# Optimization experiments

Hardware: AMD Instinct MI355X
Metric: run time of the kernel (lower is better)

## Reference

```python
import jax, jax.numpy as jnp
import numpy as np

B, S, D, H = 2, 2048, 1024, 16
DK = D // H


def setup_inputs() -> dict:
    key = jax.random.key(0)
    ks = jax.random.split(key, 12)
    k_init = 1.0 / np.sqrt(D)  # torch Linear-style uniform bound used in the module
    def lin(kw, kb):
        W = jax.random.uniform(kw, (D, D), jnp.float32, -k_init, k_init)
        b = jax.random.uniform(kb, (D,), jnp.float32, -k_init, k_init)
        return W, b
    Wq, bq = lin(ks[0], ks[1])
    Wk, bk = lin(ks[2], ks[3])
    Wv, bv = lin(ks[4], ks[5])
    Wo, bo = lin(ks[6], ks[7])
    query = jax.random.normal(ks[8], (B, S, D), jnp.float32)
    key_t = jax.random.normal(ks[9], (B, S, D), jnp.float32)
    value = jax.random.normal(ks[10], (B, S, D), jnp.float32)
    # causal mask: 1 where attention allowed, 0 where blocked
    mask = jnp.broadcast_to(jnp.tril(jnp.ones((S, S), jnp.int32)), (B, S, S))
    return {"query": query, "key": key_t, "value": value, "mask": mask,
            "Wq": Wq, "bq": bq, "Wk": Wk, "bk": bk, "Wv": Wv, "bv": bv,
            "Wo": Wo, "bo": bo}


def reference(query, key, value, mask, Wq, bq, Wk, bk, Wv, bv, Wo, bo):
    bs = query.shape[0]
    # projections: torch Linear computes x @ W.T + b
    def proj(x, W, b):
        y = x @ W.T + b                      # [B, S, D]
        return y.reshape(bs, -1, H, DK).transpose(0, 2, 1, 3)  # [B, H, S, DK]
    q = proj(query, Wq, bq)
    k = proj(key, Wk, bk)
    v = proj(value, Wv, bv)
    scale = 1.0 / np.sqrt(DK).astype(np.float32)
    scores = jnp.einsum('bhqd,bhkd->bhqk', q, k) * scale  # [B, H, S, S]
    scores = jnp.where(mask[:, None, :, :] == 0, jnp.float32(-1e9), scores)
    p_attn = jax.nn.softmax(scores, axis=-1)
    # dropout omitted (eval mode / deterministic reference)
    x = jnp.einsum('bhqk,bhkd->bhqd', p_attn, v)          # [B, H, S, DK]
    x = x.transpose(0, 2, 1, 3).reshape(bs, -1, D)        # [B, S, D]
    return x @ Wo.T + bo
```

## Files before the change

kernel.cpp:

```cpp
#include <hip/hip_runtime.h>
#include <hip/hip_bf16.h>
#include <math.h>

#define BB 2
#define SS 2048
#define DD 1024
#define HH 16
#define DKK 64
#define NT (BB * SS)

typedef __attribute__((ext_vector_type(8))) short short8;
typedef __attribute__((ext_vector_type(4))) float f32x4;
typedef __attribute__((ext_vector_type(16))) float f32x16;

__device__ __forceinline__ unsigned short f2b(float x) {
    __hip_bfloat16 h = __float2bfloat16(x);
    unsigned short u; __builtin_memcpy(&u, &h, 2); return u;
}
__device__ __forceinline__ unsigned pack2(float a, float b) {
    return (unsigned)f2b(a) | ((unsigned)f2b(b) << 16);
}

struct CastAll {
    const float* src[7];
    unsigned short* dst[7];
};

__global__ __launch_bounds__(256)
void cast_all(CastAll a) {
    const int tid0 = blockIdx.x * 256 + threadIdx.x;
    const int stride = gridDim.x * 256;
    #pragma unroll
    for (int s = 0; s < 7; ++s) {
        const int n4 = (s < 3) ? (NT * DD / 4) : (DD * DD / 4);
        const float* __restrict__ src = a.src[s];
        unsigned short* __restrict__ dst = a.dst[s];
        for (int i = tid0; i < n4; i += stride) {
            const float4 v = reinterpret_cast<const float4*>(src)[i];
            ushort4 o;
            o.x = f2b(v.x); o.y = f2b(v.y); o.z = f2b(v.z); o.w = f2b(v.w);
            reinterpret_cast<ushort4*>(dst)[i] = o;
        }
    }
}

template <int MODE>
__device__ __forceinline__ void gemm_body(const unsigned short* __restrict__ A,
                                          const unsigned short* __restrict__ W,
                                          const float* __restrict__ bias,
                                          void* __restrict__ Cv,
                                          int bm, int bn, int N, int K) {
    __shared__ __align__(16) unsigned char sA[128 * 128];
    __shared__ __align__(16) unsigned char sB[128 * 128];

    const int tid = threadIdx.x;
    const int l = tid & 63;
    const int w = tid >> 6;
    const int wr = w >> 1, wc = w & 1;
    const int g = l >> 4, li = l & 15;
    const int lrow = l >> 3;
    const int lcol = (l & 7) * 8;

    f32x4 acc[4][4];
    #pragma unroll
    for (int i = 0; i < 4; ++i)
        #pragma unroll
        for (int jj = 0; jj < 4; ++jj) {
            acc[i][jj][0] = 0.f; acc[i][jj][1] = 0.f;
            acc[i][jj][2] = 0.f; acc[i][jj][3] = 0.f;
        }

    for (int kt = 0; kt < K; kt += 64) {
        #pragma unroll
        for (int c = 0; c < 4; ++c) {
            const int row0 = w * 32 + c * 8;
            const unsigned short* gA = A + (size_t)(bm + row0 + lrow) * K + kt + lcol;
            __builtin_amdgcn_global_load_lds(
                (const __attribute__((address_space(1))) unsigned int*)gA,
                (__attribute__((address_space(3))) unsigned int*)&sA[row0 * 128],
                16, 0, 0);
            const unsigned short* gB = W + (size_t)(bn + row0 + lrow) * K + kt + lcol;
            __builtin_amdgcn_global_load_lds(
                (const __attribute__((address_space(1))) unsigned int*)gB,
                (__attribute__((address_space(3))) unsigned int*)&sB[row0 * 128],
                16, 0, 0);
        }
        __syncthreads();

        #pragma unroll
        for (int kb = 0; kb < 2; ++kb) {
            const int chb = (g + kb * 4) * 16;
            short8 af[4], bfr[4];
            #pragma unroll
            for (int mi = 0; mi < 4; ++mi)
                af[mi] = *reinterpret_cast<const short8*>(
                    &sA[(wr * 64 + mi * 16 + li) * 128 + chb]);
            #pragma unroll
            for (int ni = 0; ni < 4; ++ni)
                bfr[ni] = *reinterpret_cast<const short8*>(
                    &sB[(wc * 64 + ni * 16 + li) * 128 + chb]);
            #pragma unroll
            for (int mi = 0; mi < 4; ++mi)
                #pragma unroll
                for (int ni = 0; ni < 4; ++ni)
                    acc[mi][ni] = __builtin_amdgcn_mfma_f32_16x16x32_bf16(af[mi], bfr[ni], acc[mi][ni], 0, 0, 0);
        }
        __syncthreads();
    }

    #pragma unroll
    for (int ni = 0; ni < 4; ++ni) {
        const int col = bn + wc * 64 + ni * 16 + li;
        const float bv = bias[col];
        if constexpr (MODE == 2) {
            const int hh = col >> 6, d = col & 63;
            const int bb = bm >> 11;
            unsigned short* vt = (unsigned short*)Cv;
            #pragma unroll
            for (int mi = 0; mi < 4; ++mi) {
                const int srow0 = (bm & (SS - 1)) + wr * 64 + mi * 16 + g * 4;
                ushort4 pk4;
                pk4.x = f2b(acc[mi][ni][0] + bv);
                pk4.y = f2b(acc[mi][ni][1] + bv);
                pk4.z = f2b(acc[mi][ni][2] + bv);
                pk4.w = f2b(acc[mi][ni][3] + bv);
                *reinterpret_cast<ushort4*>(
                    &vt[(size_t)((bb * 16 + hh) * 64 + d) * SS + srow0]) = pk4;
            }
        } else {
            #pragma unroll
            for (int mi = 0; mi < 4; ++mi) {
                const int row0 = bm + wr * 64 + mi * 16 + g * 4;
                #pragma unroll
                for (int r = 0; r < 4; ++r) {
                    const float v = acc[mi][ni][r] + bv;
                    if constexpr (MODE == 0)
                        ((unsigned short*)Cv)[(size_t)(row0 + r) * N + col] = f2b(v);
                    else
                        ((float*)Cv)[(size_t)(row0 + r) * N + col] = v;
                }
            }
        }
    }
}

struct QKVArgs {
    const unsigned short* A[3];
    const unsigned short* W[3];
    const float* bias[3];
    unsigned short* C[2];
    unsigned short* vt;
};

__global__ __launch_bounds__(256)
void gemm_qkv(QKVArgs args) {
    const int bid = blockIdx.x;
    const int i = (bid & 7) * 96 + (bid >> 3);
    const int z = i >> 8;
    const int rem = i & 255;
    const int by = rem >> 3, bx = rem & 7;
    if (z == 2)
        gemm_body<2>(args.A[2], args.W[2], args.bias[2], args.vt, by * 128, bx * 128, DD, DD);
    else
        gemm_body<0>(args.A[z], args.W[z], args.bias[z], args.C[z], by * 128, bx * 128, DD, DD);
}

__global__ __launch_bounds__(256)
void gemm_out(const unsigned short* __restrict__ A, const unsigned short* __restrict__ W,
              const float* __restrict__ bias, float* __restrict__ C) {
    const int bid = blockIdx.x;
    const int i = (bid & 7) * 32 + (bid >> 3);
    const int by = i >> 3, bx = i & 7;
    gemm_body<1>(A, W, bias, C, by * 128, bx * 128, DD, DD);
}

__global__ __launch_bounds__(256)
void attn_mfma(const unsigned short* __restrict__ Q,
               const unsigned short* __restrict__ Kb,
               const unsigned short* __restrict__ Vt,
               unsigned short* __restrict__ X) {
    __shared__ __align__(16) unsigned char sK[128 * 128];
    __shared__ __align__(16) unsigned char sV[64 * 256];

    const int bid = blockIdx.x;
    const int xcd = bid & 7;
    const int idx = bid >> 3;
    const int j   = 15 - (idx >> 2);
    const int bh  = xcd * 4 + (idx & 3);
    const int b = bh >> 4, h = bh & 15;

    const int tid = threadIdx.x, l = tid & 63, w = tid >> 6;
    const int h5 = l >> 5, q5 = l & 31;
    const int col0 = h * DKK;
    const int qbase = j * 128 + w * 32;
    const float scale = 0.125f;

    short8 qf[4];
    {
        const unsigned short* qp = Q + (size_t)(b * SS + qbase + q5) * DD + col0;
        #pragma unroll
        for (int s = 0; s < 4; ++s)
            qf[s] = *reinterpret_cast<const short8*>(&qp[(2 * s + h5) * 8]);
    }

    f32x16 accO[2];
    #pragma unroll
    for (int d0 = 0; d0 < 2; ++d0)
        #pragma unroll
        for (int r = 0; r < 16; ++r) accO[d0][r] = 0.f;
    float m = -INFINITY, lsum = 0.f;

    for (int kt = 0; kt <= j; ++kt) {
        {
            const unsigned short* krow = Kb + (size_t)(b * SS + kt * 128) * DD + col0;
            #pragma unroll
            for (int i = 0; i < 4; ++i) {
                const int row = w * 32 + i * 8 + (l >> 3);
                const int cj = l & 7;
                __builtin_amdgcn_global_load_lds(
                    (const __attribute__((address_space(1))) unsigned int*)
                        (krow + (size_t)row * DD + ((cj ^ (row & 7)) << 3)),
                    (__attribute__((address_space(3))) unsigned int*)&sK[w * 4096 + i * 1024],
                    16, 0, 0);
            }
            const unsigned short* vrow = Vt + (size_t)(bh * 64) * SS + kt * 128;
            #pragma unroll
            for (int i = 0; i < 4; ++i) {
                const int d = w * 16 + i * 4 + (l >> 4);
                const int cj = l & 15;
                __builtin_amdgcn_global_load_lds(
                    (const __attribute__((address_space(1))) unsigned int*)
                        (vrow + (size_t)d * SS + ((cj ^ (d & 15)) << 3)),
                    (__attribute__((address_space(3))) unsigned int*)&sV[w * 4096 + i * 1024],
                    16, 0, 0);
            }
        }
        __syncthreads();

        const bool diag = (kt == j);
        const int fact = diag ? w : 3;

        f32x16 accS[4];
        __builtin_amdgcn_s_setprio(1);
        #pragma unroll
        for (int f = 0; f < 4; ++f) {
            if (f <= fact) {
                #pragma unroll
                for (int r = 0; r < 16; ++r) accS[f][r] = 0.f;
                #pragma unroll
                for (int s = 0; s < 4; ++s) {
                    const short8 kf = *reinterpret_cast<const short8*>(
                        &sK[(f * 32 + q5) * 128 + (((2 * s + h5) ^ (q5 & 7)) << 4)]);
                    accS[f] = __builtin_amdgcn_mfma_f32_32x32x16_bf16(kf, qf[s], accS[f], 0, 0, 0);
                }
            }
        }
        __builtin_amdgcn_s_setprio(0);

        float tmax = -INFINITY;
        #pragma unroll
        for (int f = 0; f < 4; ++f) {
            if (f <= fact) {
                #pragma unroll
                for (int r = 0; r < 16; ++r) {
                    float v = accS[f][r] * scale;
                    if (diag && f == w) {
                        const int off = (r & 3) + 8 * (r >> 2) + 4 * h5;
                        if (off > q5) v = -3e38f;
                    }
                    accS[f][r] = v;
                    tmax = fmaxf(tmax, v);
                }
            }
        }
        tmax = fmaxf(tmax, __shfl_xor(tmax, 32));

        if (!__all(tmax <= m)) {
            const float mn = fmaxf(m, tmax);
            const float corr = __expf(m - mn);
            lsum *= corr;
            #pragma unroll
            for (int r = 0; r < 16; ++r) {
                const int rowloc = (r & 3) + 8 * (r >> 2) + 4 * h5;
                const float cr = __shfl(corr, rowloc | (l & 32));
                accO[0][r] *= cr;
                accO[1][r] *= cr;
            }
            m = mn;
        }

        float psum = 0.f;
        unsigned pk[32];
        #pragma unroll
        for (int f = 0; f < 4; ++f) {
            if (f <= fact) {
                #pragma unroll
                for (int i2 = 0; i2 < 8; ++i2) {
                    const float pa = __expf(accS[f][2 * i2] - m);
                    const float pb = __expf(accS[f][2 * i2 + 1] - m);
                    psum += pa + pb;
                    pk[f * 8 + i2] = pack2(pa, pb);
                }
            }
        }
        psum += __shfl_xor(psum, 32);
        lsum += psum;

        const int smax = diag ? (2 * w + 1) : 7;
        __builtin_amdgcn_s_setprio(1);
        #pragma unroll
        for (int s = 0; s < 8; ++s) {
            if (s <= smax) {
                const int fb = (s >> 1) * 8 + (s & 1) * 4;
                const unsigned sendA = h5 ? pk[fb + 0] : pk[fb + 2];
                const unsigned sendB = h5 ? pk[fb + 1] : pk[fb + 3];
                const unsigned rA = __shfl_xor(sendA, 32);
                const unsigned rB = __shfl_xor(sendB, 32);
                union { unsigned u[4]; short8 s8; } pf;
                pf.u[0] = h5 ? rA : pk[fb + 0];
                pf.u[1] = h5 ? rB : pk[fb + 1];
                pf.u[2] = h5 ? pk[fb + 2] : rA;
                pf.u[3] = h5 ? pk[fb + 3] : rB;
                #pragma unroll
                for (int d0 = 0; d0 < 2; ++d0) {
                    const short8 vf = *reinterpret_cast<const short8*>(
                        &sV[(d0 * 32 + q5) * 256 + (((2 * s + h5) ^ (q5 & 15)) << 4)]);
                    accO[d0] = __builtin_amdgcn_mfma_f32_32x32x16_bf16(pf.s8, vf, accO[d0], 0, 0, 0);
                }
            }
        }
        __builtin_amdgcn_s_setprio(0);
        __syncthreads();
    }

    const float invl = 1.f / lsum;
    #pragma unroll
    for (int r = 0; r < 16; ++r) {
        const int rowloc = (r & 3) + 8 * (r >> 2) + 4 * h5;
        const float iv = __shfl(invl, rowloc | (l & 32));
        const size_t qrow = (size_t)(b * SS + qbase + rowloc) * DD + col0;
        #pragma unroll
        for (int d0 = 0; d0 < 2; ++d0)
            X[qrow + d0 * 32 + q5] = f2b(accO[d0][r] * iv);
    }
}

extern "C" void kernel_launch(void* const* d_in, const int* in_sizes, int n_in,
                              void* d_out, int out_size, void* d_ws, size_t ws_size,
                              hipStream_t stream) {
    const float* query = (const float*)d_in[0];
    const float* key   = (const float*)d_in[1];
    const float* value = (const float*)d_in[2];
    const float* Wq = (const float*)d_in[4];
    const float* bq = (const float*)d_in[5];
    const float* Wk = (const float*)d_in[6];
    const float* bk = (const float*)d_in[7];
    const float* Wv = (const float*)d_in[8];
    const float* bv = (const float*)d_in[9];
    const float* Wo = (const float*)d_in[10];
    const float* bo = (const float*)d_in[11];
    float* out = (float*)d_out;

    unsigned short* ws16 = (unsigned short*)d_ws;
    const size_t TOK = (size_t)NT * DD;
    const size_t WSZ = (size_t)DD * DD;
    unsigned short* qb  = ws16;
    unsigned short* kb  = ws16 + TOK;
    unsigned short* vt  = ws16 + 2 * TOK;
    unsigned short* xb  = ws16 + 3 * TOK;
    unsigned short* xqb = ws16 + 4 * TOK;
    unsigned short* xkb = ws16 + 5 * TOK;
    unsigned short* xvb = ws16 + 6 * TOK;
    unsigned short* wqb = ws16 + 7 * TOK;
    unsigned short* wkb = wqb + WSZ;
    unsigned short* wvb = wkb + WSZ;
    unsigned short* wob = wvb + WSZ;

    CastAll ca;
    ca.src[0] = query; ca.dst[0] = xqb;
    ca.src[1] = key;   ca.dst[1] = xkb;
    ca.src[2] = value; ca.dst[2] = xvb;
    ca.src[3] = Wq;    ca.dst[3] = wqb;
    ca.src[4] = Wk;    ca.dst[4] = wkb;
    ca.src[5] = Wv;    ca.dst[5] = wvb;
    ca.src[6] = Wo;    ca.dst[6] = wob;
    cast_all<<<2048, 256, 0, stream>>>(ca);

    QKVArgs args;
    args.A[0] = xqb; args.A[1] = xkb; args.A[2] = xvb;
    args.W[0] = wqb; args.W[1] = wkb; args.W[2] = wvb;
    args.bias[0] = bq; args.bias[1] = bk; args.bias[2] = bv;
    args.C[0] = qb;  args.C[1] = kb;  args.vt = vt;
    gemm_qkv<<<768, 256, 0, stream>>>(args);

    attn_mfma<<<512, 256, 0, stream>>>(qb, kb, vt, xb);

    gemm_out<<<256, 256, 0, stream>>>(xb, wob, bo, out);
}
```

Before: 273.8 us.

## Split causal attention into KV chunks with a separate merge kernel

The single causal attention kernel is replaced by a split-KV scheme. Each query tile's KV range is cut into chunks of up to four tiles, giving 1280 work items of roughly equal size instead of 512 blocks whose work grows with query position. Each chunk writes an unnormalized bf16 partial output plus its row max and sum to workspace that is reused from the cast buffers. A new merge kernel then rescales and combines the partials into X. This aims to fix load imbalance and tail effects across CUs, at the cost of an extra launch, extra global traffic for partials, and bf16 rounding of the unnormalized partials. It also adds a minimum-occupancy hint to the launch bounds.

```diff
diff --git a/kernel.cpp b/kernel.cpp
--- a/kernel.cpp
+++ b/kernel.cpp
@@ -8,6 +8,8 @@
 #define HH 16
 #define DKK 64
 #define NT (BB * SS)
+#define NCHUNK 1280
+#define CPB 40
 
 typedef __attribute__((ext_vector_type(8))) short short8;
 typedef __attribute__((ext_vector_type(4))) float f32x4;
@@ -16,6 +18,9 @@
 __device__ __forceinline__ unsigned short f2b(float x) {
     __hip_bfloat16 h = __float2bfloat16(x);
     unsigned short u; __builtin_memcpy(&u, &h, 2); return u;
+}
+__device__ __forceinline__ float b2f(unsigned short u) {
+    union { unsigned u; float f; } c; c.u = ((unsigned)u) << 16; return c.f;
 }
 __device__ __forceinline__ unsigned pack2(float a, float b) {
     return (unsigned)f2b(a) | ((unsigned)f2b(b) << 16);
@@ -174,19 +179,25 @@
     gemm_body<1>(A, W, bias, C, by * 128, bx * 128, DD, DD);
 }
 
-__global__ __launch_bounds__(256)
-void attn_mfma(const unsigned short* __restrict__ Q,
+__global__ __launch_bounds__(256, 3)
+void attn_part(const unsigned short* __restrict__ Q,
                const unsigned short* __restrict__ Kb,
                const unsigned short* __restrict__ Vt,
-               unsigned short* __restrict__ X) {
+               unsigned short* __restrict__ Opart,
+               float* __restrict__ ML) {
     __shared__ __align__(16) unsigned char sK[128 * 128];
     __shared__ __align__(16) unsigned char sV[64 * 256];
 
     const int bid = blockIdx.x;
     const int xcd = bid & 7;
-    const int idx = bid >> 3;
-    const int j   = 15 - (idx >> 2);
-    const int bh  = xcd * 4 + (idx & 3);
+    const int slot = bid >> 3;
+    const int bh = xcd * 4 + slot / CPB;
+    const int cidx = (CPB - 1) - (slot % CPB);
+    int j = 0, rem = cidx;
+    while (rem >= ((j >> 2) + 1)) { rem -= (j >> 2) + 1; ++j; }
+    const int c = rem;
+    const int kt0 = 4 * c;
+    const int kt1 = (4 * c + 3 < j) ? (4 * c + 3) : j;
     const int b = bh >> 4, h = bh & 15;
 
     const int tid = threadIdx.x, l = tid & 63, w = tid >> 6;
@@ -210,7 +221,7 @@
         for (int r = 0; r < 16; ++r) accO[d0][r] = 0.f;
     float m = -INFINITY, lsum = 0.f;
 
-    for (int kt = 0; kt <= j; ++kt) {
+    for (int kt = kt0; kt <= kt1; ++kt) {
         {
             const unsigned short* krow = Kb + (size_t)(b * SS + kt * 128) * DD + col0;
             #pragma unroll
@@ -333,15 +344,78 @@
         __syncthreads();
     }
 
-    const float invl = 1.f / lsum;
     #pragma unroll
     for (int r = 0; r < 16; ++r) {
         const int rowloc = (r & 3) + 8 * (r >> 2) + 4 * h5;
-        const float iv = __shfl(invl, rowloc | (l & 32));
-        const size_t qrow = (size_t)(b * SS + qbase + rowloc) * DD + col0;
+        const int qrow = w * 32 + rowloc;
         #pragma unroll
         for (int d0 = 0; d0 < 2; ++d0)
-            X[qrow + d0 * 32 + q5] = f2b(accO[d0][r] * iv);
+            Opart[(size_t)bid * 8192 + qrow * 64 + d0 * 32 + q5] = f2b(accO[d0][r]);
+    }
+    if (h5 == 0) {
+        ML[bid * 256 + w * 32 + q5] = m;
+        ML[bid * 256 + 128 + w * 32 + q5] = lsum;
+    }
+}
+
+__global__ __launch_bounds__(256)
+void attn_merge(const unsigned short* __restrict__ Opart,
+                const float* __restrict__ ML,
+                unsigned short* __restrict__ X) {
+    const int bid = blockIdx.x;
+    const int xcd = bid & 7, s = bid >> 3;
+    const int bh = xcd * 4 + (s >> 4);
+    const int j = s & 15;
+    const int b = bh >> 4, h = bh & 15;
+    const int a = j >> 2, bb = j & 3;
+    const int offj = (a + 1) * (2 * a + bb);
+    const int nc = a + 1;
+    const int tid = threadIdx.x;
+    const int q = tid >> 1, dh = (tid & 1) * 32;
+
+    float mc[4], lc[4];
+    float M = -INFINITY;
+    #pragma unroll
+    for (int cc = 0; cc < 4; ++cc) {
+        if (cc < nc) {
+            const int slot = (bh & 3) * CPB + (CPB - 1) - (offj + cc);
+            const int gb = slot * 8 + xcd;
+            mc[cc] = ML[gb * 256 + q];
+            lc[cc] = ML[gb * 256 + 128 + q];
+            M = fmaxf(M, mc[cc]);
+        } else { mc[cc] = -INFINITY; lc[cc] = 0.f; }
+    }
+
+    float L = 0.f;
+    float o[32];
+    #pragma unroll
+    for (int e = 0; e < 32; ++e) o[e] = 0.f;
+    #pragma unroll
+    for (int cc = 0; cc < 4; ++cc) {
+        if (cc < nc) {
+            const int slot = (bh & 3) * CPB + (CPB - 1) - (offj + cc);
+            const int gb = slot * 8 + xcd;
+            const float wgt = __expf(mc[cc] - M);
+            L += lc[cc] * wgt;
+            const unsigned short* op = Opart + (size_t)gb * 8192 + q * 64 + dh;
+            #pragma unroll
+            for (int v = 0; v < 4; ++v) {
+                const short8 pv = *reinterpret_cast<const short8*>(&op[v * 8]);
+                #pragma unroll
+                for (int e = 0; e < 8; ++e)
+                    o[v * 8 + e] += wgt * b2f((unsigned short)pv[e]);
+            }
+        }
+    }
+
+    const float inv = 1.f / L;
+    unsigned short* xp = X + (size_t)(b * SS + j * 128 + q) * DD + h * DKK + dh;
+    #pragma unroll
+    for (int v = 0; v < 4; ++v) {
+        short8 o8;
+        #pragma unroll
+        for (int e = 0; e < 8; ++e) o8[e] = (short)f2b(o[v * 8 + e] * inv);
+        *reinterpret_cast<short8*>(&xp[v * 8]) = o8;
     }
 }
 
@@ -376,6 +450,9 @@
     unsigned short* wvb = wkb + WSZ;
     unsigned short* wob = wvb + WSZ;
 
+    unsigned short* opart = xqb;
+    float* ml = (float*)wqb;
+
     CastAll ca;
     ca.src[0] = query; ca.dst[0] = xqb;
     ca.src[1] = key;   ca.dst[1] = xkb;
@@ -393,7 +470,8 @@
     args.C[0] = qb;  args.C[1] = kb;  args.vt = vt;
     gemm_qkv<<<768, 256, 0, stream>>>(args);
 
-    attn_mfma<<<512, 256, 0, stream>>>(qb, kb, vt, xb);
+    attn_part<<<NCHUNK, 256, 0, stream>>>(qb, kb, vt, opart, ml);
+    attn_merge<<<512, 256, 0, stream>>>(opart, ml, xb);
 
     gemm_out<<<256, 256, 0, stream>>>(xb, wob, bo, out);
 }
```

After: 290.2 us. 1.06x slower.

## Drop LDS staging in attention; read K/V fragments directly from global

Applied to the files above, without the earlier changes.

The attention kernel no longer stages K and V tiles in shared memory with global_load_lds and block barriers. Each wave now loads its MFMA operand fragments straight from global memory, relying on L1/L2 caching. Blocks shrink to two waves (1024 blocks of 128 threads), with per-wave causal tile counts and removed setprio hints. This removes barrier stalls and LDS traffic and lets the two waves of a block progress independently. The cost is more global/L2 traffic and uncoalesced strided row loads, since K rows are reread by every wave.

```diff
diff --git a/kernel.cpp b/kernel.cpp
--- a/kernel.cpp
+++ b/kernel.cpp
@@ -174,25 +174,25 @@
     gemm_body<1>(A, W, bias, C, by * 128, bx * 128, DD, DD);
 }
 
-__global__ __launch_bounds__(256)
+__global__ __launch_bounds__(128)
 void attn_mfma(const unsigned short* __restrict__ Q,
                const unsigned short* __restrict__ Kb,
                const unsigned short* __restrict__ Vt,
                unsigned short* __restrict__ X) {
-    __shared__ __align__(16) unsigned char sK[128 * 128];
-    __shared__ __align__(16) unsigned char sV[64 * 256];
-
     const int bid = blockIdx.x;
     const int xcd = bid & 7;
-    const int idx = bid >> 3;
-    const int j   = 15 - (idx >> 2);
-    const int bh  = xcd * 4 + (idx & 3);
+    const int slot = bid >> 3;
+    const int bh = xcd * 4 + (slot & 3);
+    const int jg2 = 31 - (slot >> 2);
     const int b = bh >> 4, h = bh & 15;
 
     const int tid = threadIdx.x, l = tid & 63, w = tid >> 6;
     const int h5 = l >> 5, q5 = l & 31;
+    const int jq = jg2 * 2 + w;
+    const int g = jq >> 2;
+    const int dfrag = jq & 3;
+    const int qbase = jq * 32;
     const int col0 = h * DKK;
-    const int qbase = j * 128 + w * 32;
     const float scale = 0.125f;
 
     short8 qf[4];
@@ -203,6 +203,9 @@
             qf[s] = *reinterpret_cast<const short8*>(&qp[(2 * s + h5) * 8]);
     }
 
+    const unsigned short* kbase = Kb + (size_t)(b * SS) * DD + col0;
+    const unsigned short* vbase = Vt + (size_t)(bh * 64) * SS;
+
     f32x16 accO[2];
     #pragma unroll
     for (int d0 = 0; d0 < 2; ++d0)
@@ -210,52 +213,24 @@
         for (int r = 0; r < 16; ++r) accO[d0][r] = 0.f;
     float m = -INFINITY, lsum = 0.f;
 
-    for (int kt = 0; kt <= j; ++kt) {
-        {
-            const unsigned short* krow = Kb + (size_t)(b * SS + kt * 128) * DD + col0;
-            #pragma unroll
-            for (int i = 0; i < 4; ++i) {
-                const int row = w * 32 + i * 8 + (l >> 3);
-                const int cj = l & 7;
-                __builtin_amdgcn_global_load_lds(
-                    (const __attribute__((address_space(1))) unsigned int*)
-                        (krow + (size_t)row * DD + ((cj ^ (row & 7)) << 3)),
-                    (__attribute__((address_space(3))) unsigned int*)&sK[w * 4096 + i * 1024],
-                    16, 0, 0);
-            }
-            const unsigned short* vrow = Vt + (size_t)(bh * 64) * SS + kt * 128;
-            #pragma unroll
-            for (int i = 0; i < 4; ++i) {
-                const int d = w * 16 + i * 4 + (l >> 4);
-                const int cj = l & 15;
-                __builtin_amdgcn_global_load_lds(
-                    (const __attribute__((address_space(1))) unsigned int*)
-                        (vrow + (size_t)d * SS + ((cj ^ (d & 15)) << 3)),
-                    (__attribute__((address_space(3))) unsigned int*)&sV[w * 4096 + i * 1024],
-                    16, 0, 0);
-            }
-        }
-        __syncthreads();
-
-        const bool diag = (kt == j);
-        const int fact = diag ? w : 3;
+    for (int kt = 0; kt <= g; ++kt) {
+        const bool diag = (kt == g);
+        const int fact = diag ? dfrag : 3;
 
         f32x16 accS[4];
-        __builtin_amdgcn_s_setprio(1);
         #pragma unroll
         for (int f = 0; f < 4; ++f) {
             if (f <= fact) {
                 #pragma unroll
                 for (int r = 0; r < 16; ++r) accS[f][r] = 0.f;
+                const unsigned short* krow = kbase + (size_t)(kt * 128 + f * 32 + q5) * DD;
                 #pragma unroll
                 for (int s = 0; s < 4; ++s) {
-                    const short8 kf = *reinterpret_cast<const short8*>(
-                        &sK[(f * 32 + q5) * 128 + (((2 * s + h5) ^ (q5 & 7)) << 4)]);
+                    const short8 kf = *reinterpret_cast<const short8*>(&krow[(2 * s + h5) * 8]);
                     accS[f] = __builtin_amdgcn_mfma_f32_32x32x16_bf16(kf, qf[s], accS[f], 0, 0, 0);
                 }
             }
         }
-        __builtin_amdgcn_s_setprio(0);
 
         float tmax = -INFINITY;
         #pragma unroll
@@ -264,7 +239,7 @@
                 #pragma unroll
                 for (int r = 0; r < 16; ++r) {
                     float v = accS[f][r] * scale;
-                    if (diag && f == w) {
+                    if (diag && f == dfrag) {
                         const int off = (r & 3) + 8 * (r >> 2) + 4 * h5;
                         if (off > q5) v = -3e38f;
                     }
@@ -306,8 +281,7 @@
         psum += __shfl_xor(psum, 32);
         lsum += psum;
 
-        const int smax = diag ? (2 * w + 1) : 7;
-        __builtin_amdgcn_s_setprio(1);
+        const int smax = diag ? (2 * dfrag + 1) : 7;
         #pragma unroll
         for (int s = 0; s < 8; ++s) {
             if (s <= smax) {
@@ -324,13 +298,11 @@
                 #pragma unroll
                 for (int d0 = 0; d0 < 2; ++d0) {
                     const short8 vf = *reinterpret_cast<const short8*>(
-                        &sV[(d0 * 32 + q5) * 256 + (((2 * s + h5) ^ (q5 & 15)) << 4)]);
+                        &vbase[(size_t)(d0 * 32 + q5) * SS + kt * 128 + (2 * s + h5) * 8]);
                     accO[d0] = __builtin_amdgcn_mfma_f32_32x32x16_bf16(pf.s8, vf, accO[d0], 0, 0, 0);
                 }
             }
         }
-        __builtin_amdgcn_s_setprio(0);
-        __syncthreads();
     }
 
     const float invl = 1.f / lsum;
@@ -393,7 +365,7 @@
     args.C[0] = qb;  args.C[1] = kb;  args.vt = vt;
     gemm_qkv<<<768, 256, 0, stream>>>(args);
 
-    attn_mfma<<<512, 256, 0, stream>>>(qb, kb, vt, xb);
+    attn_mfma<<<1024, 128, 0, stream>>>(qb, kb, vt, xb);
 
     gemm_out<<<256, 256, 0, stream>>>(xb, wob, bo, out);
 }
```

Result: slower. 294.3 us (+7.5%).
